# Optimization experiments

Hardware: AMD Instinct MI355X
Metric: run time of the kernel (lower is better)

## Reference

```python
import jax, jax.numpy as jnp
import numpy as np

B, L, E, H = 4, 256, 128, 8
NU, NT = 512, 256
D = E // H


def _mha(q_in, k_in, v_in, in_w, in_b, out_w, out_b):
    # torch nn.MultiheadAttention (batch_first) math
    Wq, Wk, Wv = jnp.split(in_w, 3, axis=0)
    bq, bk, bv = jnp.split(in_b, 3)
    Bq, Lq, _ = q_in.shape
    q = (q_in @ Wq.T + bq).reshape(Bq, Lq, H, D)
    k = (k_in @ Wk.T + bk).reshape(Bq, -1, H, D)
    v = (v_in @ Wv.T + bv).reshape(Bq, -1, H, D)
    a = jax.nn.softmax(jnp.einsum('bqhd,bkhd->bhqk', q, k) / np.sqrt(D), axis=-1)
    o = jnp.einsum('bhqk,bkhd->bqhd', a, v).reshape(Bq, Lq, E)
    return o @ out_w.T + out_b


def setup_inputs() -> dict:
    key = jax.random.key(0)
    ks = jax.random.split(key, 12)
    s = 0.05
    return {
        'UUMat': jax.random.normal(ks[0], (B, NU, E - 2), jnp.float32),
        'DUMat': jax.random.normal(ks[1], (B, L, E), jnp.float32),
        'TAMat': jax.random.normal(ks[2], (B, NT, E), jnp.float32),
        'CIMat': jax.random.normal(ks[3], (B, NU, 2 * L), jnp.float32),
        'uu_in_w': jax.random.normal(ks[4], (3 * E, E), jnp.float32) * s,
        'uu_in_b': jnp.zeros((3 * E,), jnp.float32),
        'uu_out_w': jax.random.normal(ks[5], (E, E), jnp.float32) * s,
        'uu_out_b': jnp.zeros((E,), jnp.float32),
        'ta_in_w': jax.random.normal(ks[6], (3 * E, E), jnp.float32) * s,
        'ta_in_b': jnp.zeros((3 * E,), jnp.float32),
        'ta_out_w': jax.random.normal(ks[7], (E, E), jnp.float32) * s,
        'ta_out_b': jnp.zeros((E,), jnp.float32),
        'du_in_w': jax.random.normal(ks[8], (3 * E, E), jnp.float32) * s,
        'du_in_b': jnp.zeros((3 * E,), jnp.float32),
        'du_out_w': jax.random.normal(ks[9], (E, E), jnp.float32) * s,
        'du_out_b': jnp.zeros((E,), jnp.float32),
        'dim_w': jax.random.normal(ks[10], (E, 3 * E), jnp.float32) * s,
        'dim_b': jnp.zeros((E,), jnp.float32),
        'bn_gamma': jnp.ones((E,), jnp.float32),
        'bn_beta': jnp.zeros((E,), jnp.float32),
    }


def reference(UUMat, DUMat, TAMat, CIMat,
              uu_in_w, uu_in_b, uu_out_w, uu_out_b,
              ta_in_w, ta_in_b, ta_out_w, ta_out_b,
              du_in_w, du_in_b, du_out_w, du_out_b,
              dim_w, dim_b, bn_gamma, bn_beta):
    # --- UU2DU: vectorized over the original per-l Python loop ---
    # CIVec_l = stack(CIMat[:,:,l], CIMat[:,:,l+L]) -> build all l at once
    ci = jnp.stack([CIMat[:, :, :L], CIMat[:, :, L:2 * L]], axis=-1)  # [B,N,L,2]
    ci = jnp.transpose(ci, (0, 2, 1, 3))                              # [B,L,N,2]
    uu = jnp.broadcast_to(UUMat[:, None], (B, L, NU, E - 2))
    kv = jnp.concatenate([uu, ci], axis=-1)                           # [B,L,N,E]
    Wq, Wk, Wv = jnp.split(uu_in_w, 3, axis=0)
    bq, bk, bv = jnp.split(uu_in_b, 3)
    q = (DUMat @ Wq.T + bq).reshape(B, L, H, D)       # query length 1 per step l
    k = (kv @ Wk.T + bk).reshape(B, L, NU, H, D)
    v = (kv @ Wv.T + bv).reshape(B, L, NU, H, D)
    a = jax.nn.softmax(jnp.einsum('blhd,blnhd->blhn', q, k) / np.sqrt(D), axis=-1)
    uu2du = jnp.einsum('blhn,blnhd->blhd', a, v).reshape(B, L, E) @ uu_out_w.T + uu_out_b

    ta2du = _mha(DUMat, TAMat, TAMat, ta_in_w, ta_in_b, ta_out_w, ta_out_b)
    du2du = _mha(DUMat, DUMat, DUMat, du_in_w, du_in_b, du_out_w, du_out_b)

    cat = jnp.concatenate([uu2du, ta2du, du2du], axis=-1)  # [B,L,3E]
    y = cat @ dim_w.T + dim_b                              # [B,L,E]

    # BatchNorm1d over channel E (training-mode batch stats over B and L)
    mean = y.mean(axis=(0, 1))
    var = y.var(axis=(0, 1))
    y = (y - mean) / jnp.sqrt(var + 1e-5) * bn_gamma + bn_beta
    return jax.nn.relu(y)
```

## Files before the change

kernel.cpp:

```cpp
#include <hip/hip_runtime.h>


struct PreArgs {
    const float* x[9]; const float* W[9]; const float* bia[9]; float* out[9];
    int Kdim[9]; int transNb[9];
    const float* CIMat; float* cit;
    const float* dim_w; const float* dim_b;
    const float* uu_ow; const float* uu_ob;
    const float* ta_ow; const float* ta_ob;
    const float* du_ow; const float* du_ob;
    float* Cuu; float* Cta; float* Cdu; float* bcomb;
    float* gstat;
};

__global__ __launch_bounds__(256) void pre_fused(PreArgs A)
{
    __shared__ __align__(16) float smem[2048];
    int bid = blockIdx.x, tid = threadIdx.x;
    if (bid == 0)
        for (int i = tid; i < 16 * 256; i += 256) A.gstat[i] = 0.f;

    if (bid < 704) {
        int task, mblk;
        if (bid < 448) { task = bid >> 6; mblk = bid & 63; }
        else { int r = bid - 448; task = 7 + (r >> 7); mblk = r & 127; }
        int Kd = A.Kdim[task];
        const float* x = A.x[task];
        int m0 = mblk * 16;
        if (Kd == 128) {
            const float4* x4 = (const float4*)(x + (size_t)m0 * 128);
            ((float4*)smem)[tid] = x4[tid];
            ((float4*)smem)[tid + 256] = x4[tid + 256];
        } else {
            for (int i = tid; i < 2048; i += 256) {
                int r = i >> 7, c = i & 127;
                smem[i] = (c < Kd) ? x[(size_t)(m0 + r) * Kd + c] : 0.f;
            }
        }
        __syncthreads();
        int e = tid & 127, half = tid >> 7;
        int r0 = half * 8;
        const float4* w4 = (const float4*)(A.W[task] + (size_t)e * 128);
        const float4* xs4 = (const float4*)smem;
        float acc[8];
        float bv = A.bia[task][e];
#pragma unroll
        for (int r = 0; r < 8; ++r) acc[r] = bv;
#pragma unroll 8
        for (int c = 0; c < 32; ++c) {
            float4 w = w4[c];
#pragma unroll
            for (int r = 0; r < 8; ++r) {
                float4 xv = xs4[(r0 + r) * 32 + c];
                acc[r] += w.x * xv.x + w.y * xv.y + w.z * xv.z + w.w * xv.w;
            }
        }
        int nb = A.transNb[task];
        float* op = A.out[task];
        if (nb == 0) {
#pragma unroll
            for (int r = 0; r < 8; ++r)
                op[(size_t)(m0 + r0 + r) * 128 + e] = acc[r];
        } else {
            int b = m0 / nb, nloc = m0 - b * nb;
            float* o = op + ((size_t)b * 128 + e) * nb + nloc + r0;
            float4 v0 = { acc[0], acc[1], acc[2], acc[3] };
            float4 v1 = { acc[4], acc[5], acc[6], acc[7] };
            *(float4*)o = v0;
            *(float4*)(o + 4) = v1;
        }
    } else if (bid < 1728) {
        int tb = bid - 704;
        int b = tb >> 8, tt = tb & 255;
        int n0 = (tt >> 4) * 32, c0 = (tt & 15) * 32;
        float (*tile)[33] = (float(*)[33])smem;
        int tx = tid & 31, ty = tid >> 5;
        const float* src = A.CIMat + (size_t)b * 262144;
        float* dst = A.cit + (size_t)b * 262144;
#pragma unroll
        for (int i = ty; i < 32; i += 8)
            tile[i][tx] = src[(size_t)(n0 + i) * 512 + c0 + tx];
        __syncthreads();
#pragma unroll
        for (int i = ty; i < 32; i += 8)
            dst[(size_t)(c0 + i) * 512 + n0 + tx] = tile[tx][i];
    } else {
        float* ds = smem;
        float* red = smem + 384;
        int e = bid - 1728, k = tid;
        if (k < 128) {
            ds[k]       = A.dim_w[(size_t)e * 384 + k];
            ds[128 + k] = A.dim_w[(size_t)e * 384 + 128 + k];
            ds[256 + k] = A.dim_w[(size_t)e * 384 + 256 + k];
        }
        __syncthreads();
        if (k < 128) {
            float cu = 0.f, ct = 0.f, cd = 0.f;
#pragma unroll 4
            for (int j = 0; j < 128; ++j) {
                cu += ds[j]       * A.uu_ow[(size_t)j * 128 + k];
                ct += ds[128 + j] * A.ta_ow[(size_t)j * 128 + k];
                cd += ds[256 + j] * A.du_ow[(size_t)j * 128 + k];
            }
            A.Cuu[(size_t)e * 128 + k] = cu;
            A.Cta[(size_t)e * 128 + k] = ct;
            A.Cdu[(size_t)e * 128 + k] = cd;
            red[k] = ds[k] * A.uu_ob[k] + ds[128 + k] * A.ta_ob[k] + ds[256 + k] * A.du_ob[k];
        }
        __syncthreads();
        for (int off = 64; off; off >>= 1) {
            if (k < off) red[k] += red[k + off];
            __syncthreads();
        }
        if (k == 0) A.bcomb[e] = A.dim_b[e] + red[0];
    }
}

struct AttnArgs {
    const float* qd; const float* kbaseT; const float* vbase; const float* cit;
    const float* qta; const float* ktaT; const float* vta;
    const float* qdu; const float* kduT; const float* vdu;
    const float* uu_in_w;
    float* ouu; float* ota; float* odu;
};

__global__ __launch_bounds__(256) void attn_kernel(AttnArgs A)
{
    __shared__ __align__(16) float smem[4608];
    int bid = blockIdx.x, tid = threadIdx.x;
    int xcd = bid & 7, idx = bid >> 3;
    int b = xcd >> 1, half = xcd & 1;
    int t = half * 384 + idx;

    if (t < 256) {
        int kind = t >> 7;
        int u = t & 127;
        int hg = u >> 5, lt = u & 31;
        int l0 = lt * 8, bl0 = b * 256 + l0;
        const float* q  = kind ? A.qdu  : A.qta;
        const float* kT = kind ? A.kduT : A.ktaT;
        const float* v  = kind ? A.vdu  : A.vta;
        float* o        = kind ? A.odu  : A.ota;
        float* qs  = smem;
        float* sc  = smem + 256;
        float* den = smem + 4352;
        {
            int l = tid >> 5, d = tid & 31;
            qs[l * 32 + d] = q[(size_t)(bl0 + l) * 128 + hg * 32 + d];
        }
        __syncthreads();
        {
            int n = tid;
            const float* kp = kT + ((size_t)b * 128 + hg * 32) * 256 + n;
            float acc[8][2];
#pragma unroll
            for (int l = 0; l < 8; ++l) { acc[l][0] = 0.f; acc[l][1] = 0.f; }
#pragma unroll 8
            for (int d = 0; d < 32; ++d) {
                float kv = kp[(size_t)d * 256];
                int hl = d >> 4;
#pragma unroll
                for (int l = 0; l < 8; ++l) acc[l][hl] += qs[l * 32 + d] * kv;
            }
#pragma unroll
            for (int hl = 0; hl < 2; ++hl)
#pragma unroll
                for (int l = 0; l < 8; ++l)
                    sc[(hl * 8 + l) * 256 + n] = acc[l][hl] * 0.25f;
        }
        __syncthreads();
        {
            int g = tid >> 4, j = tid & 15;
            float* row = sc + g * 256;
            float mx = -1e30f;
#pragma unroll 4
            for (int n = j; n < 256; n += 16) mx = fmaxf(mx, row[n]);
#pragma unroll
            for (int off = 8; off; off >>= 1) mx = fmaxf(mx, __shfl_down(mx, off, 16));
            mx = __shfl(mx, 0, 16);
            float s = 0.f;
#pragma unroll 4
            for (int n = j; n < 256; n += 16) {
                float ev = __expf(row[n] - mx);
                row[n] = ev; s += ev;
            }
#pragma unroll
            for (int off = 8; off; off >>= 1) s += __shfl_down(s, off, 16);
            if (j == 0) den[g] = s;
        }
        __syncthreads();
        {
            int col = tid & 31, l = tid >> 5;
            int colglob = hg * 32 + col;
            int g = (col >> 4) * 8 + l;
            const float* vcol = v + (size_t)b * 256 * 128 + colglob;
            const float* p = sc + g * 256;
            float acc = 0.f;
#pragma unroll 8
            for (int n = 0; n < 256; ++n) acc += p[n] * vcol[(size_t)n * 128];
            o[(size_t)(bl0 + l) * 128 + colglob] = acc / den[g];
        }
    } else {
        int u = t - 256;
        int hg = u >> 7, lt = u & 127;
        int l0 = lt * 2, bl0 = b * 256 + l0;
        float* qs    = smem;
        float* sc    = smem + 64;
        float* ci0s  = smem + 2112;
        float* ci1s  = smem + 3136;
        float* vpart = smem + 4160;
        float* qkA   = smem + 4416;
        float* qkB   = qkA + 4;
        float* den   = qkB + 4;
        float* hs0   = den + 4;
        float* hs1   = hs0 + 4;
        if (tid < 64) {
            int l = tid >> 5, d = tid & 31;
            qs[l * 32 + d] = A.qd[(size_t)(bl0 + l) * 128 + hg * 32 + d];
        }
        {
            ((float4*)ci0s)[tid] = ((const float4*)(A.cit + ((size_t)b * 512 + l0) * 512))[tid];
            ((float4*)ci1s)[tid] = ((const float4*)(A.cit + ((size_t)b * 512 + 256 + l0) * 512))[tid];
        }
        __syncthreads();
        if (tid < 4) {
            int hl = tid >> 1, l = tid & 1;
            float a = 0.f, c = 0.f;
#pragma unroll
            for (int d = 0; d < 16; ++d) {
                float qv = qs[l * 32 + hl * 16 + d];
                int wr = 128 + hg * 32 + hl * 16 + d;
                a += qv * A.uu_in_w[(size_t)wr * 128 + 126];
                c += qv * A.uu_in_w[(size_t)wr * 128 + 127];
            }
            qkA[tid] = a; qkB[tid] = c;
        }
        __syncthreads();
        {
            const float* kp = A.kbaseT + ((size_t)b * 128 + hg * 32) * 512 + tid;
            float acc[2][2][2];
#pragma unroll
            for (int r = 0; r < 2; ++r)
#pragma unroll
                for (int l = 0; l < 2; ++l) { acc[r][l][0] = 0.f; acc[r][l][1] = 0.f; }
#pragma unroll 8
            for (int d = 0; d < 32; ++d) {
                float kv0 = kp[(size_t)d * 512];
                float kv1 = kp[(size_t)d * 512 + 256];
                int hl = d >> 4;
#pragma unroll
                for (int l = 0; l < 2; ++l) {
                    float qv = qs[l * 32 + d];
                    acc[0][l][hl] += qv * kv0;
                    acc[1][l][hl] += qv * kv1;
                }
            }
#pragma unroll
            for (int r = 0; r < 2; ++r) {
                int n = tid + r * 256;
#pragma unroll
                for (int l = 0; l < 2; ++l) {
                    float c0 = ci0s[l * 512 + n], c1 = ci1s[l * 512 + n];
#pragma unroll
                    for (int hl = 0; hl < 2; ++hl) {
                        int g = hl * 2 + l;
                        sc[g * 512 + n] = (acc[r][l][hl] + c0 * qkA[g] + c1 * qkB[g]) * 0.25f;
                    }
                }
            }
        }
        __syncthreads();
        {
            int g = tid >> 6, j = tid & 63;
            int l = g & 1;
            float* row = sc + g * 512;
            const float* c0r = ci0s + l * 512;
            const float* c1r = ci1s + l * 512;
            float mx = -1e30f;
#pragma unroll
            for (int n = j; n < 512; n += 64) mx = fmaxf(mx, row[n]);
#pragma unroll
            for (int off = 32; off; off >>= 1) mx = fmaxf(mx, __shfl_down(mx, off, 64));
            mx = __shfl(mx, 0, 64);
            float s = 0.f, a0 = 0.f, a1 = 0.f;
#pragma unroll
            for (int n = j; n < 512; n += 64) {
                float ev = __expf(row[n] - mx);
                row[n] = ev;
                s += ev; a0 += ev * c0r[n]; a1 += ev * c1r[n];
            }
#pragma unroll
            for (int off = 32; off; off >>= 1) {
                s  += __shfl_down(s, off, 64);
                a0 += __shfl_down(a0, off, 64);
                a1 += __shfl_down(a1, off, 64);
            }
            if (j == 0) { den[g] = s; hs0[g] = a0; hs1[g] = a1; }
        }
        __syncthreads();
        {
            int col = tid & 31, l = (tid >> 5) & 1, nq = tid >> 6;
            int colglob = hg * 32 + col;
            int g = (col >> 4) * 2 + l;
            const float* vcol = A.vbase + ((size_t)b * 512 + nq * 128) * 128 + colglob;
            const float* p = sc + g * 512 + nq * 128;
            float acc = 0.f;
#pragma unroll 8
            for (int n = 0; n < 128; ++n) acc += p[n] * vcol[(size_t)n * 128];
            vpart[nq * 64 + l * 32 + col] = acc;
        }
        __syncthreads();
        if (tid < 64) {
            int col = tid & 31, l = tid >> 5;
            int colglob = hg * 32 + col;
            int g = (col >> 4) * 2 + l;
            float sum = vpart[tid] + vpart[64 + tid] + vpart[128 + tid] + vpart[192 + tid];
            float wv126 = A.uu_in_w[(size_t)(256 + colglob) * 128 + 126];
            float wv127 = A.uu_in_w[(size_t)(256 + colglob) * 128 + 127];
            A.ouu[(size_t)(bl0 + l) * 128 + colglob] =
                (sum + hs0[g] * wv126 + hs1[g] * wv127) / den[g];
        }
    }
}

__global__ __launch_bounds__(256) void epilogue_kernel(
    const float* __restrict__ ouu, const float* __restrict__ ota,
    const float* __restrict__ odu,
    const float* __restrict__ Cuu, const float* __restrict__ Cta,
    const float* __restrict__ Cdu, const float* __restrict__ bcomb,
    float* __restrict__ y, float* __restrict__ gstat)
{
    __shared__ __align__(16) float xs[4 * 384];
    __shared__ float vp[512];
    int m0 = blockIdx.x * 4;
    int tid = threadIdx.x;
    for (int i = tid; i < 1536; i += 256) {
        int r = i / 384, c = i - r * 384;
        float v;
        if (c < 128)      v = ouu[(size_t)(m0 + r) * 128 + c];
        else if (c < 256) v = ota[(size_t)(m0 + r) * 128 + c - 128];
        else              v = odu[(size_t)(m0 + r) * 128 + c - 256];
        xs[i] = v;
    }
    __syncthreads();
    int e = tid & 127, half = tid >> 7;
    const float4* cu4 = (const float4*)(Cuu + (size_t)e * 128);
    const float4* ct4 = (const float4*)(Cta + (size_t)e * 128);
    const float4* cd4 = (const float4*)(Cdu + (size_t)e * 128);
    const float4* xs4 = (const float4*)xs;
    float bc = bcomb[e];
    float acc[2] = { bc, bc };
    int r0 = half * 2;
#pragma unroll 4
    for (int c = 0; c < 32; ++c) {
        float4 a = cu4[c], bb = ct4[c], d = cd4[c];
#pragma unroll
        for (int rr = 0; rr < 2; ++rr) {
            float4 xu = xs4[(r0 + rr) * 96 + c];
            float4 xt = xs4[(r0 + rr) * 96 + 32 + c];
            float4 xd = xs4[(r0 + rr) * 96 + 64 + c];
            acc[rr] += a.x * xu.x + a.y * xu.y + a.z * xu.z + a.w * xu.w
                     + bb.x * xt.x + bb.y * xt.y + bb.z * xt.z + bb.w * xt.w
                     + d.x * xd.x + d.y * xd.y + d.z * xd.z + d.w * xd.w;
        }
    }
#pragma unroll
    for (int rr = 0; rr < 2; ++rr)
        y[(size_t)(m0 + r0 + rr) * 128 + e] = acc[rr];
    vp[tid] = acc[0] + acc[1];
    vp[256 + tid] = acc[0] * acc[0] + acc[1] * acc[1];
    __syncthreads();
    if (tid < 128) {
        float* gs = gstat + (blockIdx.x & 15) * 256;
        atomicAdd(gs + tid, vp[tid] + vp[tid + 128]);
        atomicAdd(gs + 128 + tid, vp[256 + tid] + vp[256 + tid + 128]);
    }
}

__global__ __launch_bounds__(256) void bn_apply(
    const float* __restrict__ y, const float* __restrict__ gstat,
    const float* __restrict__ gamma, const float* __restrict__ beta,
    float* __restrict__ out)
{
    int gid = blockIdx.x * 256 + threadIdx.x;
    int c0 = (gid & 31) * 4;
    float4 v = ((const float4*)y)[gid];
    float r[4] = { v.x, v.y, v.z, v.w };
#pragma unroll
    for (int k = 0; k < 4; ++k) {
        int c = c0 + k;
        float s = 0.f, s2 = 0.f;
#pragma unroll
        for (int cp = 0; cp < 16; ++cp) {
            s  += gstat[cp * 256 + c];
            s2 += gstat[cp * 256 + 128 + c];
        }
        float mean = s * (1.f / 1024.f);
        float var = s2 * (1.f / 1024.f) - mean * mean;
        float inv = rsqrtf(var + 1e-5f);
        r[k] = fmaxf((r[k] - mean) * inv * gamma[c] + beta[c], 0.f);
    }
    float4 ov = { r[0], r[1], r[2], r[3] };
    ((float4*)out)[gid] = ov;
}

extern "C" void kernel_launch(void* const* d_in, const int* in_sizes, int n_in,
                              void* d_out, int out_size, void* d_ws, size_t ws_size,
                              hipStream_t stream)
{
    (void)in_sizes; (void)n_in; (void)out_size; (void)ws_size;
    const float* UUMat    = (const float*)d_in[0];
    const float* DUMat    = (const float*)d_in[1];
    const float* TAMat    = (const float*)d_in[2];
    const float* CIMat    = (const float*)d_in[3];
    const float* uu_in_w  = (const float*)d_in[4];
    const float* uu_in_b  = (const float*)d_in[5];
    const float* uu_out_w = (const float*)d_in[6];
    const float* uu_out_b = (const float*)d_in[7];
    const float* ta_in_w  = (const float*)d_in[8];
    const float* ta_in_b  = (const float*)d_in[9];
    const float* ta_out_w = (const float*)d_in[10];
    const float* ta_out_b = (const float*)d_in[11];
    const float* du_in_w  = (const float*)d_in[12];
    const float* du_in_b  = (const float*)d_in[13];
    const float* du_out_w = (const float*)d_in[14];
    const float* du_out_b = (const float*)d_in[15];
    const float* dim_w    = (const float*)d_in[16];
    const float* dim_b    = (const float*)d_in[17];
    const float* bn_g     = (const float*)d_in[18];
    const float* bn_b     = (const float*)d_in[19];

    const int BL = 1024, BN = 2048;
    float* ws = (float*)d_ws;
    float* gstat  = ws; ws += 16 * 256;
    float* cit    = ws; ws += (size_t)4 * 512 * 512;
    float* qd     = ws; ws += (size_t)BL * 128;
    float* kbaseT = ws; ws += (size_t)BN * 128;
    float* vbase  = ws; ws += (size_t)BN * 128;
    float* qta    = ws; ws += (size_t)BL * 128;
    float* ktaT   = ws; ws += (size_t)BL * 128;
    float* vta    = ws; ws += (size_t)BL * 128;
    float* qdu    = ws; ws += (size_t)BL * 128;
    float* kduT   = ws; ws += (size_t)BL * 128;
    float* vdu    = ws; ws += (size_t)BL * 128;
    float* ouu    = ws; ws += (size_t)BL * 128;
    float* ota    = ws; ws += (size_t)BL * 128;
    float* odu    = ws; ws += (size_t)BL * 128;
    float* yy     = ws; ws += (size_t)BL * 128;
    float* Cuu    = ws; ws += 128 * 128;
    float* Cta    = ws; ws += 128 * 128;
    float* Cdu    = ws; ws += 128 * 128;
    float* bcomb  = ws; ws += 128;

    PreArgs P;
    P.x[0] = DUMat; P.W[0] = uu_in_w;             P.bia[0] = uu_in_b;       P.out[0] = qd;     P.Kdim[0] = 128; P.transNb[0] = 0;
    P.x[1] = DUMat; P.W[1] = ta_in_w;             P.bia[1] = ta_in_b;       P.out[1] = qta;    P.Kdim[1] = 128; P.transNb[1] = 0;
    P.x[2] = TAMat; P.W[2] = ta_in_w + 128 * 128; P.bia[2] = ta_in_b + 128; P.out[2] = ktaT;   P.Kdim[2] = 128; P.transNb[2] = 256;
    P.x[3] = TAMat; P.W[3] = ta_in_w + 256 * 128; P.bia[3] = ta_in_b + 256; P.out[3] = vta;    P.Kdim[3] = 128; P.transNb[3] = 0;
    P.x[4] = DUMat; P.W[4] = du_in_w;             P.bia[4] = du_in_b;       P.out[4] = qdu;    P.Kdim[4] = 128; P.transNb[4] = 0;
    P.x[5] = DUMat; P.W[5] = du_in_w + 128 * 128; P.bia[5] = du_in_b + 128; P.out[5] = kduT;   P.Kdim[5] = 128; P.transNb[5] = 256;
    P.x[6] = DUMat; P.W[6] = du_in_w + 256 * 128; P.bia[6] = du_in_b + 256; P.out[6] = vdu;    P.Kdim[6] = 128; P.transNb[6] = 0;
    P.x[7] = UUMat; P.W[7] = uu_in_w + 128 * 128; P.bia[7] = uu_in_b + 128; P.out[7] = kbaseT; P.Kdim[7] = 126; P.transNb[7] = 512;
    P.x[8] = UUMat; P.W[8] = uu_in_w + 256 * 128; P.bia[8] = uu_in_b + 256; P.out[8] = vbase;  P.Kdim[8] = 126; P.transNb[8] = 0;
    P.CIMat = CIMat; P.cit = cit;
    P.dim_w = dim_w; P.dim_b = dim_b;
    P.uu_ow = uu_out_w; P.uu_ob = uu_out_b;
    P.ta_ow = ta_out_w; P.ta_ob = ta_out_b;
    P.du_ow = du_out_w; P.du_ob = du_out_b;
    P.Cuu = Cuu; P.Cta = Cta; P.Cdu = Cdu; P.bcomb = bcomb;
    P.gstat = gstat;

    AttnArgs T;
    T.qd = qd; T.kbaseT = kbaseT; T.vbase = vbase; T.cit = cit;
    T.qta = qta; T.ktaT = ktaT; T.vta = vta;
    T.qdu = qdu; T.kduT = kduT; T.vdu = vdu;
    T.uu_in_w = uu_in_w;
    T.ouu = ouu; T.ota = ota; T.odu = odu;

    hipLaunchKernelGGL(pre_fused, dim3(1856), dim3(256), 0, stream, P);
    hipLaunchKernelGGL(attn_kernel, dim3(3072), dim3(256), 0, stream, T);
    hipLaunchKernelGGL(epilogue_kernel, dim3(256), dim3(256), 0, stream,
                       ouu, ota, odu, Cuu, Cta, Cdu, bcomb, yy, gstat);
    hipLaunchKernelGGL(bn_apply, dim3(128), dim3(256), 0, stream,
                       yy, gstat, bn_g, bn_b, (float*)d_out);
}
```

Measured before the change: 184.7 us.

## Drop softmax max pass, fuse exp into scores, vectorize PV with split-N

The max-reduction pass of the softmax is removed and exp is applied directly when scores are written to shared memory, leaving a single sum pass. The P·V stage now reads V as float4 and splits the key dimension across thread groups, with partial sums reduced through shared memory. Score rows are padded (260/516) to avoid LDS bank conflicts. Skipping max subtraction risks overflow if scores grow large, and it trades an extra barrier and more shared memory for better load width and parallelism.

```diff
diff --git a/kernel.cpp b/kernel.cpp
--- a/kernel.cpp
+++ b/kernel.cpp
@@ -124,9 +124,12 @@
     float* ouu; float* ota; float* odu;
 };
 
+#define SCP 260
+#define SCPU 516
+
 __global__ __launch_bounds__(256) void attn_kernel(AttnArgs A)
 {
-    __shared__ __align__(16) float smem[4608];
+    __shared__ __align__(16) float smem[5472];
     int bid = blockIdx.x, tid = threadIdx.x;
     int xcd = bid & 7, idx = bid >> 3;
     int b = xcd >> 1, half = xcd & 1;
@@ -141,9 +144,10 @@
         const float* kT = kind ? A.kduT : A.ktaT;
         const float* v  = kind ? A.vdu  : A.vta;
         float* o        = kind ? A.odu  : A.ota;
-        float* qs  = smem;
-        float* sc  = smem + 256;
-        float* den = smem + 4352;
+        float* qs    = smem;
+        float* sc    = smem + 256;
+        float* vpart = smem + 4416;
+        float* den   = smem + 5440;
         {
             int l = tid >> 5, d = tid & 31;
             qs[l * 32 + d] = q[(size_t)(bl0 + l) * 128 + hg * 32 + d];
@@ -166,39 +170,42 @@
             for (int hl = 0; hl < 2; ++hl)
 #pragma unroll
                 for (int l = 0; l < 8; ++l)
-                    sc[(hl * 8 + l) * 256 + n] = acc[l][hl] * 0.25f;
+                    sc[(hl * 8 + l) * SCP + n] = __expf(acc[l][hl] * 0.25f);
         }
         __syncthreads();
         {
             int g = tid >> 4, j = tid & 15;
-            float* row = sc + g * 256;
-            float mx = -1e30f;
-#pragma unroll 4
-            for (int n = j; n < 256; n += 16) mx = fmaxf(mx, row[n]);
-#pragma unroll
-            for (int off = 8; off; off >>= 1) mx = fmaxf(mx, __shfl_down(mx, off, 16));
-            mx = __shfl(mx, 0, 16);
+            const float* row = sc + g * SCP;
             float s = 0.f;
 #pragma unroll 4
-            for (int n = j; n < 256; n += 16) {
-                float ev = __expf(row[n] - mx);
-                row[n] = ev; s += ev;
-            }
+            for (int n = j; n < 256; n += 16) s += row[n];
 #pragma unroll
             for (int off = 8; off; off >>= 1) s += __shfl_down(s, off, 16);
             if (j == 0) den[g] = s;
         }
         __syncthreads();
         {
+            int col4 = tid & 7, l = (tid >> 3) & 7, nh = tid >> 6;
+            const float4* v4 = (const float4*)v + (size_t)b * 256 * 32 + hg * 8 + col4;
+            const float* p = sc + ((col4 >> 2) * 8 + l) * SCP;
+            float4 a4 = { 0.f, 0.f, 0.f, 0.f };
+            int n0 = nh * 64;
+#pragma unroll 8
+            for (int n = n0; n < n0 + 64; ++n) {
+                float pv = p[n];
+                float4 vv = v4[(size_t)n * 32];
+                a4.x += pv * vv.x; a4.y += pv * vv.y;
+                a4.z += pv * vv.z; a4.w += pv * vv.w;
+            }
+            ((float4*)vpart)[nh * 64 + l * 8 + col4] = a4;
+        }
+        __syncthreads();
+        {
             int col = tid & 31, l = tid >> 5;
-            int colglob = hg * 32 + col;
-            int g = (col >> 4) * 8 + l;
-            const float* vcol = v + (size_t)b * 256 * 128 + colglob;
-            const float* p = sc + g * 256;
-            float acc = 0.f;
-#pragma unroll 8
-            for (int n = 0; n < 256; ++n) acc += p[n] * vcol[(size_t)n * 128];
-            o[(size_t)(bl0 + l) * 128 + colglob] = acc / den[g];
+            int col4 = col >> 2, j = col & 3;
+            int base = (l * 8 + col4) * 4 + j;
+            float sum = vpart[base] + vpart[256 + base] + vpart[512 + base] + vpart[768 + base];
+            o[(size_t)(bl0 + l) * 128 + hg * 32 + col] = sum / den[(col >> 4) * 8 + l];
         }
     } else {
         int u = t - 256;
@@ -206,10 +213,10 @@
         int l0 = lt * 2, bl0 = b * 256 + l0;
         float* qs    = smem;
         float* sc    = smem + 64;
-        float* ci0s  = smem + 2112;
-        float* ci1s  = smem + 3136;
-        float* vpart = smem + 4160;
-        float* qkA   = smem + 4416;
+        float* ci0s  = smem + 2128;
+        float* ci1s  = smem + 3152;
+        float* vpart = smem + 4176;
+        float* qkA   = smem + 5200;
         float* qkB   = qkA + 4;
         float* den   = qkB + 4;
         float* hs0   = den + 4;
@@ -264,7 +271,8 @@
 #pragma unroll
                     for (int hl = 0; hl < 2; ++hl) {
                         int g = hl * 2 + l;
-                        sc[g * 512 + n] = (acc[r][l][hl] + c0 * qkA[g] + c1 * qkB[g]) * 0.25f;
+                        sc[g * SCPU + n] =
+                            __expf((acc[r][l][hl] + c0 * qkA[g] + c1 * qkB[g]) * 0.25f);
                     }
                 }
             }
@@ -273,20 +281,13 @@
         {
             int g = tid >> 6, j = tid & 63;
             int l = g & 1;
-            float* row = sc + g * 512;
+            const float* row = sc + g * SCPU;
             const float* c0r = ci0s + l * 512;
             const float* c1r = ci1s + l * 512;
-            float mx = -1e30f;
-#pragma unroll
-            for (int n = j; n < 512; n += 64) mx = fmaxf(mx, row[n]);
-#pragma unroll
-            for (int off = 32; off; off >>= 1) mx = fmaxf(mx, __shfl_down(mx, off, 64));
-            mx = __shfl(mx, 0, 64);
             float s = 0.f, a0 = 0.f, a1 = 0.f;
 #pragma unroll
             for (int n = j; n < 512; n += 64) {
-                float ev = __expf(row[n] - mx);
-                row[n] = ev;
+                float ev = row[n];
                 s += ev; a0 += ev * c0r[n]; a1 += ev * c1r[n];
             }
 #pragma unroll
@@ -299,22 +300,29 @@
         }
         __syncthreads();
         {
-            int col = tid & 31, l = (tid >> 5) & 1, nq = tid >> 6;
-            int colglob = hg * 32 + col;
-            int g = (col >> 4) * 2 + l;
-            const float* vcol = A.vbase + ((size_t)b * 512 + nq * 128) * 128 + colglob;
-            const float* p = sc + g * 512 + nq * 128;
-            float acc = 0.f;
+            int col4 = tid & 7, l = (tid >> 3) & 1, nh = tid >> 4;
+            const float4* v4 = (const float4*)A.vbase + (size_t)b * 512 * 32 + hg * 8 + col4;
+            const float* p = sc + ((col4 >> 2) * 2 + l) * SCPU;
+            float4 a4 = { 0.f, 0.f, 0.f, 0.f };
+            int n0 = nh * 32;
 #pragma unroll 8
-            for (int n = 0; n < 128; ++n) acc += p[n] * vcol[(size_t)n * 128];
-            vpart[nq * 64 + l * 32 + col] = acc;
+            for (int n = n0; n < n0 + 32; ++n) {
+                float pv = p[n];
+                float4 vv = v4[(size_t)n * 32];
+                a4.x += pv * vv.x; a4.y += pv * vv.y;
+                a4.z += pv * vv.z; a4.w += pv * vv.w;
+            }
+            ((float4*)vpart)[nh * 16 + l * 8 + col4] = a4;
         }
         __syncthreads();
         if (tid < 64) {
             int col = tid & 31, l = tid >> 5;
             int colglob = hg * 32 + col;
             int g = (col >> 4) * 2 + l;
-            float sum = vpart[tid] + vpart[64 + tid] + vpart[128 + tid] + vpart[192 + tid];
+            int base = (l * 8 + (col >> 2)) * 4 + (col & 3);
+            float sum = 0.f;
+#pragma unroll
+            for (int nh = 0; nh < 16; ++nh) sum += vpart[nh * 64 + base];
             float wv126 = A.uu_in_w[(size_t)(256 + colglob) * 128 + 126];
             float wv127 = A.uu_in_w[(size_t)(256 + colglob) * 128 + 127];
             A.ouu[(size_t)(bl0 + l) * 128 + colglob] =
```

Measured after the change: 186.1 us. No clear change (+0.7%).
